# Kernel optimization log

Hardware: AMD Instinct MI355X
Metric: run time of the kernel (lower is better)

Reference implementation:

```python
import jax, jax.numpy as jnp
import numpy as np

N_NODES = 50000
N_EDGES = 1600000
D_IN = 128
D_OUT = 32
ALPHA = 0.2  # LeakyReLU negative slope


def setup_inputs() -> dict:
    key = jax.random.key(0)
    k1, k2, k3, k4, k5, k6 = jax.random.split(key, 6)
    gain = float(np.sqrt(2.0))  # relu gain, xavier_normal-style scale
    X = jax.random.normal(k1, (N_NODES, D_IN), dtype=jnp.float32)
    weights = jax.random.normal(k2, (D_IN, D_OUT), dtype=jnp.float32) * (gain * np.sqrt(2.0 / (D_IN + D_OUT)))
    a0 = jax.random.normal(k3, (1, D_OUT), dtype=jnp.float32) * (gain * np.sqrt(2.0 / (1 + D_OUT)))
    a1 = jax.random.normal(k4, (1, D_OUT), dtype=jnp.float32) * (gain * np.sqrt(2.0 / (1 + D_OUT)))
    row_idx = jax.random.randint(k5, (N_EDGES,), 0, N_NODES, dtype=jnp.int32)
    col_idx = jax.random.randint(k6, (N_EDGES,), 0, N_NODES, dtype=jnp.int32)
    return {"X": X, "weights": weights, "a0": a0, "a1": a1,
            "row_idx": row_idx, "col_idx": col_idx}


def _minmax_norm(v):
    vmin = jnp.min(v)
    vmax = jnp.max(v)
    return (v - vmin) / (vmax - vmin)


def reference(X, weights, a0, a1, row_idx, col_idx):
    # X_prime = X @ W  -> [N, D]
    X_prime = X @ weights
    # Per-node partial scores; edge score e(i->j) = a0.X_prime[i] + a1.X_prime[j]
    s0 = jnp.sum(X_prime * a0, axis=-1)  # [N]
    s1 = jnp.sum(X_prime * a1, axis=-1)  # [N]
    att = s0[row_idx] + s1[col_idx]      # [E]
    # leakyrelu -> min-max normalize over all edges -> exp
    att = jax.nn.leaky_relu(att, negative_slope=ALPHA)
    att = jnp.exp(_minmax_norm(att))
    # rows_sum = SpMM(att, ones) = per-destination-row sum of edge weights
    rows_sum = jax.ops.segment_sum(att, row_idx, num_segments=N_NODES)  # [N]
    # h_prime = SpMM(att, X_prime) / rows_sum  (dropout p=0 -> identity)
    h = jax.ops.segment_sum(att[:, None] * X_prime[col_idx], row_idx,
                            num_segments=N_NODES)  # [N, D]
    return h / rows_sum[:, None]
```

## Files before the change

### kernel.cpp

```cpp
#include <hip/hip_runtime.h>
#include <hip/hip_bf16.h>
#include <math.h>

#define N_NODES 50000
#define N_EDGES 1600000
#define D_IN 128
#define D_OUT 32
#define ALPHA 0.2f

#define NB   256
#define RPB  196
#define CAP  8192
#define GST  16
#define PT   8
#define EBK  512
#define EB   (PT * EBK)
#define NEB  ((N_EDGES + EB - 1) / EB)
#define XNPB 64
#define NXB  ((N_NODES + XNPB - 1) / XNPB)
#define XLS  33

__device__ __forceinline__ int enc_f(float x) {
    int i = __float_as_int(x);
    return i >= 0 ? i : (i ^ 0x7fffffff);
}
__device__ __forceinline__ float dec_f(int k) {
    return __int_as_float(k >= 0 ? k : (k ^ 0x7fffffff));
}
__device__ __forceinline__ unsigned short f2bf(float x) {
    __hip_bfloat16 h = __float2bfloat16(x);
    return *(unsigned short*)&h;
}
__device__ __forceinline__ float bf2f(unsigned short u) {
    return __uint_as_float((unsigned)u << 16);
}

__global__ __launch_bounds__(256) void k_gemm(const float* __restrict__ X,
                                              const float* __restrict__ W,
                                              const float* __restrict__ a0,
                                              const float* __restrict__ a1,
                                              unsigned short* __restrict__ Xpb,
                                              float* __restrict__ s0,
                                              float* __restrict__ s1,
                                              int* __restrict__ gcount) {
    __shared__ float4 Wl4[1024];
    __shared__ float4 Xl4[XNPB * XLS];
    const int tid = threadIdx.x;
    if (blockIdx.x == 0) {
        int4* g4 = (int4*)gcount;
#pragma unroll
        for (int i = 0; i < NB * GST / 4 / 256; ++i)
            g4[tid + 256 * i] = make_int4(0, 0, 0, 0);
    }
    const int node0 = blockIdx.x * XNPB;
    {
        const float4* W4 = (const float4*)W;
#pragma unroll
        for (int i = 0; i < 4; ++i) Wl4[tid + 256 * i] = W4[tid + 256 * i];
        const float4* X4 = (const float4*)X + (size_t)node0 * (D_IN / 4);
        const int lim = (min(XNPB, N_NODES - node0)) * (D_IN / 4);
#pragma unroll
        for (int i = 0; i < 8; ++i) {
            const int idx = tid + 256 * i;
            const float4 v = (idx < lim) ? X4[idx]
                                         : make_float4(0.f, 0.f, 0.f, 0.f);
            Xl4[(idx >> 5) * XLS + (idx & 31)] = v;
        }
    }
    __syncthreads();
    const int g = tid >> 3;
    const int l = tid & 7;
    const float4* xr0 = &Xl4[g * XLS];
    const float4* xr1 = &Xl4[(g + 32) * XLS];
    float axA = 0.f, ayA = 0.f, azA = 0.f, awA = 0.f;
    float axB = 0.f, ayB = 0.f, azB = 0.f, awB = 0.f;
#pragma unroll 4
    for (int kk = 0; kk < D_IN / 4; ++kk) {
        const float4 xa = xr0[kk];
        const float4 xb = xr1[kk];
        const float4 w0 = Wl4[(4 * kk + 0) * 8 + l];
        const float4 w1 = Wl4[(4 * kk + 1) * 8 + l];
        const float4 w2 = Wl4[(4 * kk + 2) * 8 + l];
        const float4 w3 = Wl4[(4 * kk + 3) * 8 + l];
        axA += xa.x * w0.x + xa.y * w1.x + xa.z * w2.x + xa.w * w3.x;
        ayA += xa.x * w0.y + xa.y * w1.y + xa.z * w2.y + xa.w * w3.y;
        azA += xa.x * w0.z + xa.y * w1.z + xa.z * w2.z + xa.w * w3.z;
        awA += xa.x * w0.w + xa.y * w1.w + xa.z * w2.w + xa.w * w3.w;
        axB += xb.x * w0.x + xb.y * w1.x + xb.z * w2.x + xb.w * w3.x;
        ayB += xb.x * w0.y + xb.y * w1.y + xb.z * w2.y + xb.w * w3.y;
        azB += xb.x * w0.z + xb.y * w1.z + xb.z * w2.z + xb.w * w3.z;
        awB += xb.x * w0.w + xb.y * w1.w + xb.z * w2.w + xb.w * w3.w;
    }
    const float4 av0 = ((const float4*)a0)[l];
    const float4 av1 = ((const float4*)a1)[l];
    {
        const int node = node0 + g;
        if (node < N_NODES) {
            uint2 pk;
            pk.x = ((unsigned)f2bf(ayA) << 16) | f2bf(axA);
            pk.y = ((unsigned)f2bf(awA) << 16) | f2bf(azA);
            ((uint2*)Xpb)[(size_t)node * 8 + l] = pk;
            float v0 = axA * av0.x + ayA * av0.y + azA * av0.z + awA * av0.w;
            float v1 = axA * av1.x + ayA * av1.y + azA * av1.z + awA * av1.w;
#pragma unroll
            for (int m = 4; m >= 1; m >>= 1) {
                v0 += __shfl_xor(v0, m);
                v1 += __shfl_xor(v1, m);
            }
            if (l == 0) { s0[node] = v0; s1[node] = v1; }
        }
    }
    {
        const int node = node0 + g + 32;
        if (node < N_NODES) {
            uint2 pk;
            pk.x = ((unsigned)f2bf(ayB) << 16) | f2bf(axB);
            pk.y = ((unsigned)f2bf(awB) << 16) | f2bf(azB);
            ((uint2*)Xpb)[(size_t)node * 8 + l] = pk;
            float v0 = axB * av0.x + ayB * av0.y + azB * av0.z + awB * av0.w;
            float v1 = axB * av1.x + ayB * av1.y + azB * av1.z + awB * av1.w;
#pragma unroll
            for (int m = 4; m >= 1; m >>= 1) {
                v0 += __shfl_xor(v0, m);
                v1 += __shfl_xor(v1, m);
            }
            if (l == 0) { s0[node] = v0; s1[node] = v1; }
        }
    }
}

__global__ __launch_bounds__(512) void k_edge(const int* __restrict__ row,
                                              const int* __restrict__ col,
                                              const float* __restrict__ s0,
                                              const float* __restrict__ s1,
                                              int* __restrict__ gcount,
                                              int2* __restrict__ mm,
                                              uint2* __restrict__ gEdges) {
    __shared__ uint2 rec[EB];
    __shared__ int hist[NB];
    __shared__ int off[NB + 1];
    __shared__ int lcur[NB];
    __shared__ int gbase[NB];
    __shared__ int wse[4];
    __shared__ int smn[8], smx[8];
    const int tid = threadIdx.x;
    if (tid < NB) hist[tid] = 0;
    __syncthreads();
    const int base = blockIdx.x * EB;
    unsigned px[PT];
    float    fa[PT];
    int cnt = 0;
    int kmin = 0x7fffffff, kmax = 0x80000000;
    if (base + EB <= N_EDGES) {
#pragma unroll
        for (int i = 0; i < PT / 4; ++i) {
            const int4 r4 = ((const int4*)(row + base))[tid + i * EBK];
            const int4 c4 = ((const int4*)(col + base))[tid + i * EBK];
            const int rr[4] = {r4.x, r4.y, r4.z, r4.w};
            const int cc[4] = {c4.x, c4.y, c4.z, c4.w};
#pragma unroll
            for (int j = 0; j < 4; ++j) {
                const int r = rr[j];
                const int c = cc[j];
                float a = s0[r] + s1[c];
                a = a > 0.f ? a : ALPHA * a;
                const int k = enc_f(a);
                kmin = min(kmin, k);
                kmax = max(kmax, k);
                const unsigned b = (unsigned)r / RPB;
                const unsigned lr = (unsigned)r - b * RPB;
                px[cnt] = (b << 24) | (lr << 16) | (unsigned)c;
                fa[cnt] = a;
                ++cnt;
                atomicAdd(&hist[b], 1);
            }
        }
    } else {
#pragma unroll
        for (int i = 0; i < PT; ++i) {
            const int e = base + i * EBK + tid;
            if (e >= N_EDGES) break;
            const int r = row[e];
            const int c = col[e];
            float a = s0[r] + s1[c];
            a = a > 0.f ? a : ALPHA * a;
            const int k = enc_f(a);
            kmin = min(kmin, k);
            kmax = max(kmax, k);
            const unsigned b = (unsigned)r / RPB;
            const unsigned lr = (unsigned)r - b * RPB;
            px[cnt] = (b << 24) | (lr << 16) | (unsigned)c;
            fa[cnt] = a;
            ++cnt;
            atomicAdd(&hist[b], 1);
        }
    }
    __syncthreads();
    int h = 0, inc = 0;
    if (tid < NB) {
        h = hist[tid];
        gbase[tid] = h > 0 ? atomicAdd(&gcount[tid << 4], h) : 0;
        inc = h;
        const int lane = tid & 63;
#pragma unroll
        for (int d = 1; d < 64; d <<= 1) {
            const int u = __shfl_up(inc, d);
            if (lane >= d) inc += u;
        }
        if (lane == 63) wse[tid >> 6] = inc;
    }
    __syncthreads();
    if (tid < NB) {
        int addp = 0;
        const int wv = tid >> 6;
#pragma unroll
        for (int w = 0; w < 4; ++w)
            if (w < wv) addp += wse[w];
        const int exc = inc - h + addp;
        off[tid] = exc;
        lcur[tid] = exc;
        if (tid == NB - 1) off[NB] = inc + addp;
    }
    __syncthreads();
    for (int j = 0; j < cnt; ++j) {
        const unsigned b = px[j] >> 24;
        const int p = atomicAdd(&lcur[b], 1);
        rec[p] = make_uint2(px[j], (unsigned)__float_as_int(fa[j]));
    }
    __syncthreads();
    const int total = off[NB];
    for (int i = tid; i < total; i += EBK) {
        const uint2 e = rec[i];
        const unsigned b = e.x >> 24;
        const int pos = gbase[b] + (i - off[b]);
        if (pos < CAP) gEdges[(size_t)b * CAP + pos] = e;
    }
#pragma unroll
    for (int m = 32; m >= 1; m >>= 1) {
        kmin = min(kmin, __shfl_xor(kmin, m));
        kmax = max(kmax, __shfl_xor(kmax, m));
    }
    const int wave = tid >> 6;
    if ((tid & 63) == 0) { smn[wave] = kmin; smx[wave] = kmax; }
    __syncthreads();
    if (tid == 0) {
#pragma unroll
        for (int w = 1; w < 8; ++w) {
            kmin = min(kmin, smn[w]);
            kmax = max(kmax, smx[w]);
        }
        mm[blockIdx.x] = make_int2(kmin, kmax);
    }
}

__global__ __launch_bounds__(1024, 1) void k_bucket(const int* __restrict__ gcount,
                                                    const uint2* __restrict__ gEdges,
                                                    const unsigned short* __restrict__ Xpb,
                                                    const int2* __restrict__ mm,
                                                    float* __restrict__ out) {
    __shared__ unsigned short scol[CAP];
    __shared__ float swt[CAP];
    __shared__ int off[RPB + 1];
    __shared__ int cur[RPB];
    __shared__ int wsc[4];
    __shared__ int rmn[16], rmx[16];
    __shared__ float s_mn, s_inv;
    const int b = blockIdx.x;
    const int t = threadIdx.x;
    const int cnt = min(gcount[b << 4], CAP);
    const uint2* eb = gEdges + (size_t)b * CAP;

    int kmn = 0x7fffffff, kmx = 0x80000000;
    for (int i = t; i < NEB; i += 1024) {
        const int2 v = mm[i];
        kmn = min(kmn, v.x);
        kmx = max(kmx, v.y);
    }
#pragma unroll
    for (int m = 32; m >= 1; m >>= 1) {
        kmn = min(kmn, __shfl_xor(kmn, m));
        kmx = max(kmx, __shfl_xor(kmx, m));
    }
    if ((t & 63) == 0) { rmn[t >> 6] = kmn; rmx[t >> 6] = kmx; }
    if (t < RPB) cur[t] = 0;
    __syncthreads();
    if (t == 0) {
#pragma unroll
        for (int w = 1; w < 16; ++w) {
            kmn = min(kmn, rmn[w]);
            kmx = max(kmx, rmx[w]);
        }
        const float mn = dec_f(kmn);
        const float mx = dec_f(kmx);
        s_mn = mn;
        s_inv = 1.0f / (mx - mn);
    }
    for (int i = t; i < cnt; i += 1024)
        atomicAdd(&cur[(eb[i].x >> 16) & 0xFFu], 1);
    __syncthreads();
    int inc_s = 0, v_s = 0;
    if (t < 256) {
        v_s = (t < RPB) ? cur[t] : 0;
        inc_s = v_s;
        const int lane = t & 63;
#pragma unroll
        for (int d = 1; d < 64; d <<= 1) {
            const int u = __shfl_up(inc_s, d);
            if (lane >= d) inc_s += u;
        }
        if (lane == 63) wsc[t >> 6] = inc_s;
    }
    __syncthreads();
    if (t < 256) {
        int addp = 0;
        const int wv = t >> 6;
#pragma unroll
        for (int w = 0; w < 4; ++w)
            if (w < wv) addp += wsc[w];
        if (t < RPB) off[t] = inc_s - v_s + addp;
        if (t == 255) off[RPB] = inc_s + addp;
    }
    __syncthreads();
    if (t < RPB) cur[t] = off[t];
    __syncthreads();
    const float mn = s_mn;
    const float inv = s_inv;
    for (int i = t; i < cnt; i += 1024) {
        const uint2 e = eb[i];
        const int lr = (int)((e.x >> 16) & 0xFFu);
        const int p = atomicAdd(&cur[lr], 1);
        if (p < CAP) {
            scol[p] = (unsigned short)(e.x & 0xFFFFu);
            swt[p] = __expf((__int_as_float(e.y) - mn) * inv);
        }
    }
    __syncthreads();

    const int proc = t >> 4;
    const int d2 = t & 15;
    const unsigned* Xp32 = (const unsigned*)Xpb;
    for (int lr = proc; lr < RPB; lr += 64) {
        const int s = off[lr];
        const int e2 = off[lr + 1];
        float pa0 = 0.f, pa1 = 0.f, pa2 = 0.f, pa3 = 0.f;
        float pb0 = 0.f, pb1 = 0.f, pb2 = 0.f, pb3 = 0.f;
        float w0s = 0.f, w1s = 0.f, w2s = 0.f, w3s = 0.f;
        int i = s;
        for (; i + 3 < e2; i += 4) {
            const int c0 = scol[i];
            const int c1 = scol[i + 1];
            const int c2 = scol[i + 2];
            const int c3 = scol[i + 3];
            const float w0 = swt[i];
            const float w1 = swt[i + 1];
            const float w2 = swt[i + 2];
            const float w3 = swt[i + 3];
            const unsigned u0 = Xp32[(size_t)c0 * 16 + d2];
            const unsigned u1 = Xp32[(size_t)c1 * 16 + d2];
            const unsigned u2 = Xp32[(size_t)c2 * 16 + d2];
            const unsigned u3 = Xp32[(size_t)c3 * 16 + d2];
            pa0 += w0 * bf2f((unsigned short)(u0 & 0xFFFFu));
            pb0 += w0 * bf2f((unsigned short)(u0 >> 16));
            pa1 += w1 * bf2f((unsigned short)(u1 & 0xFFFFu));
            pb1 += w1 * bf2f((unsigned short)(u1 >> 16));
            pa2 += w2 * bf2f((unsigned short)(u2 & 0xFFFFu));
            pb2 += w2 * bf2f((unsigned short)(u2 >> 16));
            pa3 += w3 * bf2f((unsigned short)(u3 & 0xFFFFu));
            pb3 += w3 * bf2f((unsigned short)(u3 >> 16));
            w0s += w0; w1s += w1; w2s += w2; w3s += w3;
        }
        for (; i < e2; ++i) {
            const float w = swt[i];
            const unsigned u = Xp32[(size_t)scol[i] * 16 + d2];
            pa0 += w * bf2f((unsigned short)(u & 0xFFFFu));
            pb0 += w * bf2f((unsigned short)(u >> 16));
            w0s += w;
        }
        const int r = b * RPB + lr;
        if (r < N_NODES) {
            const float ws = w0s + w1s + w2s + w3s;
            float2 o;
            o.x = (pa0 + pa1 + pa2 + pa3) / ws;
            o.y = (pb0 + pb1 + pb2 + pb3) / ws;
            ((float2*)out)[(size_t)r * 16 + d2] = o;
        }
    }
}

extern "C" void kernel_launch(void* const* d_in, const int* in_sizes, int n_in,
                              void* d_out, int out_size, void* d_ws, size_t ws_size,
                              hipStream_t stream) {
    const float* X  = (const float*)d_in[0];
    const float* W  = (const float*)d_in[1];
    const float* a0 = (const float*)d_in[2];
    const float* a1 = (const float*)d_in[3];
    const int* row  = (const int*)d_in[4];
    const int* col  = (const int*)d_in[5];
    float* out = (float*)d_out;

    float* ws = (float*)d_ws;
    int*   gcount = (int*)ws + 64;
    int2*  mm = (int2*)((int*)ws + 64 + NB * GST);
    float* s0 = ws + 64 + NB * GST + 1024;
    float* s1 = s0 + 50048;
    unsigned short* Xpb = (unsigned short*)(s1 + 50048);
    uint2* gEdges = (uint2*)(s1 + 50048 + 800000);

    k_gemm<<<NXB, 256, 0, stream>>>(X, W, a0, a1, Xpb, s0, s1, gcount);
    k_edge<<<NEB, 512, 0, stream>>>(row, col, s0, s1, gcount, mm, gEdges);
    k_bucket<<<NB, 1024, 0, stream>>>(gcount, gEdges, Xpb, mm, out);
}
```

Baseline: 140.3 us.

## Read X directly from global in GEMM and halve edges per thread in edge pass

The GEMM kernel no longer stages X tiles in shared memory. Each 8-thread group now reads its node's row straight from global memory (with clamped indices), which cuts LDS use and a sync-heavy staging step. The edge kernel processes 4 edges per thread instead of 8, doubling the number of edge blocks so more work runs in parallel, and the workspace offset for s0 is enlarged to fit the larger min/max array. The direct global reads depend on L1/L2 broadcast across the 8 threads that share a row, and more edge blocks mean more global histogram/count traffic.

```diff
diff --git a/kernel.cpp b/kernel.cpp
--- a/kernel.cpp
+++ b/kernel.cpp
@@ -12,13 +12,12 @@
 #define RPB  196
 #define CAP  8192
 #define GST  16
-#define PT   8
+#define PT   4
 #define EBK  512
 #define EB   (PT * EBK)
 #define NEB  ((N_EDGES + EB - 1) / EB)
 #define XNPB 64
 #define NXB  ((N_NODES + XNPB - 1) / XNPB)
-#define XLS  33
 
 __device__ __forceinline__ int enc_f(float x) {
     int i = __float_as_int(x);
@@ -44,7 +43,6 @@
                                               float* __restrict__ s1,
                                               int* __restrict__ gcount) {
     __shared__ float4 Wl4[1024];
-    __shared__ float4 Xl4[XNPB * XLS];
     const int tid = threadIdx.x;
     if (blockIdx.x == 0) {
         int4* g4 = (int4*)gcount;
@@ -52,26 +50,20 @@
         for (int i = 0; i < NB * GST / 4 / 256; ++i)
             g4[tid + 256 * i] = make_int4(0, 0, 0, 0);
     }
-    const int node0 = blockIdx.x * XNPB;
     {
         const float4* W4 = (const float4*)W;
 #pragma unroll
         for (int i = 0; i < 4; ++i) Wl4[tid + 256 * i] = W4[tid + 256 * i];
-        const float4* X4 = (const float4*)X + (size_t)node0 * (D_IN / 4);
-        const int lim = (min(XNPB, N_NODES - node0)) * (D_IN / 4);
-#pragma unroll
-        for (int i = 0; i < 8; ++i) {
-            const int idx = tid + 256 * i;
-            const float4 v = (idx < lim) ? X4[idx]
-                                         : make_float4(0.f, 0.f, 0.f, 0.f);
-            Xl4[(idx >> 5) * XLS + (idx & 31)] = v;
-        }
     }
     __syncthreads();
     const int g = tid >> 3;
     const int l = tid & 7;
-    const float4* xr0 = &Xl4[g * XLS];
-    const float4* xr1 = &Xl4[(g + 32) * XLS];
+    const int nodeA = blockIdx.x * XNPB + g;
+    const int nodeB = nodeA + 32;
+    const float4* xr0 =
+        (const float4*)X + (size_t)min(nodeA, N_NODES - 1) * (D_IN / 4);
+    const float4* xr1 =
+        (const float4*)X + (size_t)min(nodeB, N_NODES - 1) * (D_IN / 4);
     float axA = 0.f, ayA = 0.f, azA = 0.f, awA = 0.f;
     float axB = 0.f, ayB = 0.f, azB = 0.f, awB = 0.f;
 #pragma unroll 4
@@ -94,12 +86,11 @@
     const float4 av0 = ((const float4*)a0)[l];
     const float4 av1 = ((const float4*)a1)[l];
     {
-        const int node = node0 + g;
-        if (node < N_NODES) {
+        if (nodeA < N_NODES) {
             uint2 pk;
             pk.x = ((unsigned)f2bf(ayA) << 16) | f2bf(axA);
             pk.y = ((unsigned)f2bf(awA) << 16) | f2bf(azA);
-            ((uint2*)Xpb)[(size_t)node * 8 + l] = pk;
+            ((uint2*)Xpb)[(size_t)nodeA * 8 + l] = pk;
             float v0 = axA * av0.x + ayA * av0.y + azA * av0.z + awA * av0.w;
             float v1 = axA * av1.x + ayA * av1.y + azA * av1.z + awA * av1.w;
 #pragma unroll
@@ -107,16 +98,15 @@
                 v0 += __shfl_xor(v0, m);
                 v1 += __shfl_xor(v1, m);
             }
-            if (l == 0) { s0[node] = v0; s1[node] = v1; }
+            if (l == 0) { s0[nodeA] = v0; s1[nodeA] = v1; }
         }
     }
     {
-        const int node = node0 + g + 32;
-        if (node < N_NODES) {
+        if (nodeB < N_NODES) {
             uint2 pk;
             pk.x = ((unsigned)f2bf(ayB) << 16) | f2bf(axB);
             pk.y = ((unsigned)f2bf(awB) << 16) | f2bf(azB);
-            ((uint2*)Xpb)[(size_t)node * 8 + l] = pk;
+            ((uint2*)Xpb)[(size_t)nodeB * 8 + l] = pk;
             float v0 = axB * av0.x + ayB * av0.y + azB * av0.z + awB * av0.w;
             float v1 = axB * av1.x + ayB * av1.y + azB * av1.z + awB * av1.w;
 #pragma unroll
@@ -124,7 +114,7 @@
                 v0 += __shfl_xor(v0, m);
                 v1 += __shfl_xor(v1, m);
             }
-            if (l == 0) { s0[node] = v0; s1[node] = v1; }
+            if (l == 0) { s0[nodeB] = v0; s1[nodeB] = v1; }
         }
     }
 }
@@ -152,28 +142,25 @@
     int cnt = 0;
     int kmin = 0x7fffffff, kmax = 0x80000000;
     if (base + EB <= N_EDGES) {
-#pragma unroll
-        for (int i = 0; i < PT / 4; ++i) {
-            const int4 r4 = ((const int4*)(row + base))[tid + i * EBK];
-            const int4 c4 = ((const int4*)(col + base))[tid + i * EBK];
-            const int rr[4] = {r4.x, r4.y, r4.z, r4.w};
-            const int cc[4] = {c4.x, c4.y, c4.z, c4.w};
-#pragma unroll
-            for (int j = 0; j < 4; ++j) {
-                const int r = rr[j];
-                const int c = cc[j];
-                float a = s0[r] + s1[c];
-                a = a > 0.f ? a : ALPHA * a;
-                const int k = enc_f(a);
-                kmin = min(kmin, k);
-                kmax = max(kmax, k);
-                const unsigned b = (unsigned)r / RPB;
-                const unsigned lr = (unsigned)r - b * RPB;
-                px[cnt] = (b << 24) | (lr << 16) | (unsigned)c;
-                fa[cnt] = a;
-                ++cnt;
-                atomicAdd(&hist[b], 1);
-            }
+        const int4 r4 = ((const int4*)(row + base))[tid];
+        const int4 c4 = ((const int4*)(col + base))[tid];
+        const int rr[4] = {r4.x, r4.y, r4.z, r4.w};
+        const int cc[4] = {c4.x, c4.y, c4.z, c4.w};
+#pragma unroll
+        for (int j = 0; j < 4; ++j) {
+            const int r = rr[j];
+            const int c = cc[j];
+            float a = s0[r] + s1[c];
+            a = a > 0.f ? a : ALPHA * a;
+            const int k = enc_f(a);
+            kmin = min(kmin, k);
+            kmax = max(kmax, k);
+            const unsigned b = (unsigned)r / RPB;
+            const unsigned lr = (unsigned)r - b * RPB;
+            px[cnt] = (b << 24) | (lr << 16) | (unsigned)c;
+            fa[cnt] = a;
+            ++cnt;
+            atomicAdd(&hist[b], 1);
         }
     } else {
 #pragma unroll
@@ -401,7 +388,7 @@
     float* ws = (float*)d_ws;
     int*   gcount = (int*)ws + 64;
     int2*  mm = (int2*)((int*)ws + 64 + NB * GST);
-    float* s0 = ws + 64 + NB * GST + 1024;
+    float* s0 = ws + 64 + NB * GST + 2048;
     float* s1 = s0 + 50048;
     unsigned short* Xpb = (unsigned short*)(s1 + 50048);
     uint2* gEdges = (uint2*)(s1 + 50048 + 800000);
```

Result: slower. 146.4 us (+4.4%).
